# Kernel optimization log

Hardware: AMD Instinct MI355X
Metric: run time of the kernel (lower is better)

Reference implementation:

```python
import jax, jax.numpy as jnp
import numpy as np

TEMP = 0.2
L_MAIN, L_VIEW, L_SUP, L_UNSUP = 1.0, 1.0, 1.0, 0.2
N, D, V, P, NEG, U = 100000, 256, 3, 1024, 1024, 2048


def setup_inputs() -> dict:
    key = jax.random.key(0)
    ks = jax.random.split(key, 8)
    fused_logit = jax.random.normal(ks[0], (N,), dtype=jnp.float32)
    view_logits = jax.random.normal(ks[1], (V, N), dtype=jnp.float32)
    proj = jax.random.normal(ks[2], (V, N, D), dtype=jnp.float32)
    proj = proj / jnp.linalg.norm(proj, axis=-1, keepdims=True)  # 'already normalized'
    labels = jax.random.randint(ks[3], (N,), 0, 2).astype(jnp.float32)
    train_mask = jax.random.randint(ks[4], (N,), 0, 2).astype(bool)
    train_pos_idx = jax.random.randint(ks[5], (P,), 0, N)
    train_neg_idx = jax.random.randint(ks[6], (NEG,), 0, N)
    unlabeled_idx = jax.random.randint(ks[7], (U,), 0, N)  # len == max_unsup_samples -> no subsampling
    return dict(fused_logit=fused_logit, view_logits=view_logits, proj=proj,
                labels=labels, train_mask=train_mask, train_pos_idx=train_pos_idx,
                train_neg_idx=train_neg_idx, unlabeled_idx=unlabeled_idx)


def _masked_bce(logits, labels, mask):
    # BCEWithLogitsLoss mean over masked elements (stable formulation)
    bce = jnp.maximum(logits, 0) - logits * labels + jnp.log1p(jnp.exp(-jnp.abs(logits)))
    mf = mask.astype(logits.dtype)
    return jnp.sum(bce * mf) / jnp.maximum(jnp.sum(mf), 1.0)


def _sup_contrastive(proj, pos_idx, neg_idx, temp):
    lab_idx = jnp.concatenate([pos_idx, neg_idx])
    node_labels = jnp.concatenate([jnp.ones(pos_idx.shape[0]), jnp.zeros(neg_idx.shape[0])])
    L = lab_idx.shape[0]
    Vv = proj.shape[0]
    z = proj[:, lab_idx, :].transpose(1, 0, 2)          # [L, V, D]
    zf = z.reshape(L * Vv, -1)                           # [L*V, D]
    sim = (zf @ zf.T) / temp                             # [L*V, L*V]
    sim = sim - jax.lax.stop_gradient(sim.max(axis=1, keepdims=True))
    es = jnp.exp(sim)
    node = jnp.repeat(jnp.arange(L), Vv)
    view = jnp.tile(jnp.arange(Vv), L)
    flab = jnp.repeat(node_labels, Vv)
    sn = node[:, None] == node[None, :]
    sv = view[:, None] == view[None, :]
    sl = flab[:, None] == flab[None, :]
    eye = jnp.eye(L * Vv, dtype=bool)
    pos_m = ((sn & ~sv) | (~sn & sl)) & ~eye
    neg_m = (~sn) & (~sl) & ~eye
    den_m = pos_m | neg_m
    denom = jnp.sum(es * den_m.astype(es.dtype), axis=1) + 1e-12
    posf = pos_m.astype(es.dtype)
    log_prob = -jnp.log((es * posf + 1e-12) / denom[:, None])
    pos_count = pos_m.sum(axis=1)
    loss_per_anchor = jnp.sum(log_prob * posf, axis=1) / (pos_count.astype(es.dtype) + 1e-12)
    valid = ((pos_count > 0) & (den_m.sum(axis=1) > 0)).astype(es.dtype)
    return jnp.sum(loss_per_anchor * valid) / jnp.maximum(jnp.sum(valid), 1.0)


def _unsup_consistency(proj, unl_idx, temp):
    # Vectorized form of the double python loop: full cosine-sim matrix with
    # masked denominator (all but self) and positives = same node, other views.
    Vv = proj.shape[0]
    z = proj[:, unl_idx, :].transpose(1, 0, 2)           # [U, V, D]
    Uu = z.shape[0]
    M = Uu * Vv
    zf = z.reshape(M, -1)
    zn = zf / (jnp.linalg.norm(zf, axis=1, keepdims=True) + 1e-8)
    es = jnp.exp((zn @ zn.T) / temp)                     # [M, M]
    denom = es.sum(axis=1) - jnp.diag(es) + 1e-12        # exclude self
    node = jnp.repeat(jnp.arange(Uu), Vv)
    view = jnp.tile(jnp.arange(Vv), Uu)
    pos_m = (node[:, None] == node[None, :]) & (view[:, None] != view[None, :])
    posf = pos_m.astype(es.dtype)
    log_prob = -jnp.log(es / denom[:, None])
    per_anchor = jnp.sum(log_prob * posf, axis=1) / (Vv - 1)
    return jnp.mean(per_anchor)


def reference(fused_logit, view_logits, proj, labels, train_mask,
              train_pos_idx, train_neg_idx, unlabeled_idx):
    main_loss = _masked_bce(fused_logit, labels, train_mask)
    view_loss = jnp.mean(jax.vmap(lambda lg: _masked_bce(lg, labels, train_mask))(view_logits))
    sup_loss = _sup_contrastive(proj, train_pos_idx, train_neg_idx, TEMP)
    unsup_loss = _unsup_consistency(proj, unlabeled_idx, TEMP)
    total = L_MAIN * main_loss + L_VIEW * view_loss + L_SUP * sup_loss + L_UNSUP * unsup_loss
    return jnp.stack([total, main_loss, view_loss, sup_loss, unsup_loss])
```

## Files before the change

### kernel.cpp

```cpp
#include <hip/hip_runtime.h>
#include <math.h>

typedef short short8 __attribute__((ext_vector_type(8)));
typedef float floatx4 __attribute__((ext_vector_type(4)));

#define TEMP_INV 5.0f
#define W_UNSUP 0.2f
#define NB_BCE 256
#define NSPLIT 4

static __device__ __forceinline__ unsigned short f2bf(float f) {
  unsigned int u = __float_as_uint(f);
  u += 0x7FFFu + ((u >> 16) & 1u);
  return (unsigned short)(u >> 16);
}

__device__ __forceinline__ float block_sum256(float v) {
  __shared__ float sh[4];
  for (int m = 1; m <= 32; m <<= 1) v += __shfl_xor(v, m);
  __syncthreads();
  if ((threadIdx.x & 63) == 0) sh[threadIdx.x >> 6] = v;
  __syncthreads();
  return sh[0] + sh[1] + sh[2] + sh[3];
}

__global__ void detect_kernel(const unsigned int* __restrict__ w, int nw, int* __restrict__ flag) {
  __shared__ int s_int, s_flt;
  if (threadIdx.x == 0) { s_int = 1; s_flt = 1; }
  __syncthreads();
  for (int i = threadIdx.x; i < nw; i += blockDim.x) {
    unsigned int x = w[i];
    if (x != 0u && x != 1u) s_int = 0;
    if (x != 0u && x != 0x3F800000u) s_flt = 0;
  }
  __syncthreads();
  if (threadIdx.x == 0) *flag = s_int ? 0 : (s_flt ? 1 : 2);
}

__global__ __launch_bounds__(256) void bce_kernel(
    const float* __restrict__ fused, const float* __restrict__ viewl,
    const float* __restrict__ labels, const void* __restrict__ maskp,
    const int* __restrict__ flagp, float* __restrict__ partials, int N, int V) {
  const int flag = *flagp;
  float cnt = 0.f, sm = 0.f;
  float sv[8];
  for (int v = 0; v < 8; v++) sv[v] = 0.f;
  const int Vc = V > 8 ? 8 : V;
  for (int i = blockIdx.x * blockDim.x + threadIdx.x; i < N; i += gridDim.x * blockDim.x) {
    bool m;
    if (flag == 0)      m = ((const int*)maskp)[i] != 0;
    else if (flag == 1) m = ((const float*)maskp)[i] != 0.0f;
    else                m = ((const unsigned char*)maskp)[i] != 0;
    if (!m) continue;
    float y = labels[i];
    cnt += 1.0f;
    float x = fused[i];
    sm += fmaxf(x, 0.f) - x * y + log1pf(__expf(-fabsf(x)));
    for (int v = 0; v < Vc; v++) {
      float xv = viewl[(size_t)v * N + i];
      sv[v] += fmaxf(xv, 0.f) - xv * y + log1pf(__expf(-fabsf(xv)));
    }
  }
  float tot = block_sum256(cnt);
  if (threadIdx.x == 0) partials[blockIdx.x * 16 + 0] = tot;
  tot = block_sum256(sm);
  if (threadIdx.x == 0) partials[blockIdx.x * 16 + 1] = tot;
  for (int v = 0; v < Vc; v++) {
    tot = block_sum256(sv[v]);
    if (threadIdx.x == 0) partials[blockIdx.x * 16 + 2 + v] = tot;
  }
}

__global__ __launch_bounds__(256) void gather_kernel(
    const float* __restrict__ proj, const int* __restrict__ pos_idx,
    const int* __restrict__ neg_idx, const int* __restrict__ unl_idx,
    unsigned short* __restrict__ zsup, unsigned short* __restrict__ zuns,
    float* __restrict__ dsup, float* __restrict__ duns,
    int N, int D, int V, int P, int Msup, int Muns) {
  const int prob = blockIdx.y;
  const int r = blockIdx.x;
  const int M = prob ? Muns : Msup;
  if (r >= M) return;
  const int l = r / V, v = r - l * V;
  const int idx = prob ? unl_idx[l] : (l < P ? pos_idx[l] : neg_idx[l - P]);
  const float* src = proj + ((size_t)v * N + (size_t)idx) * D;
  const int t = threadIdx.x;
  float s = 0.f;
  for (int d = t; d < D; d += blockDim.x) { float x = src[d]; s += x * x; }
  for (int m = 1; m <= 32; m <<= 1) s += __shfl_xor(s, m);
  __shared__ float sh[4];
  if ((t & 63) == 0) sh[t >> 6] = s;
  __syncthreads();
  const float n2 = sh[0] + sh[1] + sh[2] + sh[3];
  if (prob == 0) {
    for (int d = t; d < D; d += blockDim.x) zsup[(size_t)r * D + d] = f2bf(src[d]);
    if (t == 0) dsup[r] = n2 * TEMP_INV;
  } else {
    const float sc = 1.0f / (sqrtf(n2) + 1e-8f);
    for (int d = t; d < D; d += blockDim.x) zuns[(size_t)r * D + d] = f2bf(src[d] * sc);
    if (t == 0) duns[r] = n2 * sc * sc * TEMP_INV;
  }
}

__global__ __launch_bounds__(256) void sim_kernel(
    const unsigned short* __restrict__ zsup, const unsigned short* __restrict__ zuns,
    float* __restrict__ Esup, float* __restrict__ Bsup,
    float* __restrict__ Euns, float* __restrict__ Buns,
    int Msup, int Muns, int PV, int V) {
  const int prob = blockIdx.z;
  const unsigned short* __restrict__ z = prob ? zuns : zsup;
  float* __restrict__ Ep = prob ? Euns : Esup;
  float* __restrict__ Bp = prob ? Buns : Bsup;
  const int M = prob ? Muns : Msup;

  const int tid = threadIdx.x;
  const int lane = tid & 63;
  const int wave = tid >> 6;
  const int q = lane >> 4;
  const int n16 = lane & 15;

  const int rowBase = blockIdx.y * 64 + wave * 16;

  int arow = rowBase + n16; if (arow >= M) arow = M - 1;
  short8 afrag[8];
  {
    const unsigned short* zr = z + (size_t)arow * 256 + q * 8;
#pragma unroll
    for (int ks = 0; ks < 8; ks++) afrag[ks] = *(const short8*)(zr + ks * 32);
  }

  int bs[4], be[4];
#pragma unroll
  for (int r = 0; r < 4; r++) {
    int row = rowBase + q * 4 + r;
    if (row >= M) row = M - 1;
    if (prob == 0) { bs[r] = (row < PV) ? 0 : PV; be[r] = (row < PV) ? PV : M; }
    else           { int b0 = (row / V) * V; bs[r] = b0; be[r] = b0 + V; }
  }

  float Eacc[4] = {0.f, 0.f, 0.f, 0.f};
  float Bacc[4] = {0.f, 0.f, 0.f, 0.f};

  __shared__ __align__(16) unsigned short lds[64 * 264];

  int cps = ((M + NSPLIT * 64 - 1) / (NSPLIT * 64)) * 64;
  int colStart = blockIdx.x * cps;
  int colEnd = colStart + cps; if (colEnd > M) colEnd = M;

  for (int c0 = colStart; c0 < colEnd; c0 += 64) {
    __syncthreads();
#pragma unroll
    for (int cc = 0; cc < 8; cc++) {
      int chunk = cc * 256 + tid;
      int rrow = chunk >> 5;
      int off = (chunk & 31) * 8;
      int gcol = c0 + rrow;
      short8 vv = {0, 0, 0, 0, 0, 0, 0, 0};
      if (gcol < M) vv = *(const short8*)(z + (size_t)gcol * 256 + off);
      *(short8*)(&lds[rrow * 264 + off]) = vv;
    }
    __syncthreads();

#pragma unroll
    for (int cb = 0; cb < 4; cb++) {
      floatx4 acc = {0.f, 0.f, 0.f, 0.f};
      const unsigned short* bp = &lds[(cb * 16 + n16) * 264 + q * 8];
#pragma unroll
      for (int ks = 0; ks < 8; ks++) {
        short8 bfrag = *(const short8*)(bp + ks * 32);
        acc = __builtin_amdgcn_mfma_f32_16x16x32_bf16(afrag[ks], bfrag, acc, 0, 0, 0);
      }
      int j = c0 + cb * 16 + n16;
      if (j < M) {
#pragma unroll
        for (int r = 0; r < 4; r++) {
          float t = acc[r] * TEMP_INV;
          Eacc[r] += __expf(t - 5.0f);
          Bacc[r] += (j >= bs[r] && j < be[r]) ? t : 0.0f;
        }
      }
    }
  }

#pragma unroll
  for (int r = 0; r < 4; r++) {
    float e = Eacc[r], b = Bacc[r];
    for (int m = 1; m <= 8; m <<= 1) { e += __shfl_xor(e, m); b += __shfl_xor(b, m); }
    int row = rowBase + q * 4 + r;
    if (n16 == 0 && row < M) {
      Ep[(size_t)blockIdx.x * M + row] = e;
      Bp[(size_t)blockIdx.x * M + row] = b;
    }
  }
}

__global__ __launch_bounds__(256) void finalize_kernel(
    const float* __restrict__ partials,
    const float* __restrict__ Esup, const float* __restrict__ Bsup, const float* __restrict__ dsup,
    const float* __restrict__ Euns, const float* __restrict__ Buns, const float* __restrict__ duns,
    int Msup, int Muns, int PV, int P, int NEG, int V, float* __restrict__ out) {
  const int t = threadIdx.x;
  float cnt = 0.f, sm = 0.f, sv[8];
  for (int v = 0; v < 8; v++) sv[v] = 0.f;
  const int Vc = V > 8 ? 8 : V;
  for (int b = t; b < NB_BCE; b += 256) {
    cnt += partials[b * 16 + 0];
    sm  += partials[b * 16 + 1];
    for (int v = 0; v < Vc; v++) sv[v] += partials[b * 16 + 2 + v];
  }
  cnt = block_sum256(cnt);
  sm = block_sum256(sm);
  float svt = 0.f;
  for (int v = 0; v < Vc; v++) svt += block_sum256(sv[v]);
  const float denomC = fmaxf(cnt, 1.0f);
  const float main_loss = sm / denomC;
  const float view_loss = (svt / denomC) / (float)V;

  float ssup = 0.f;
  for (int row = t; row < Msup; row += 256) {
    float E = 0.f, B = 0.f;
    for (int s = 0; s < NSPLIT; s++) {
      E += Esup[(size_t)s * Msup + row];
      B += Bsup[(size_t)s * Msup + row];
    }
    float d = dsup[row];
    float dn = E - __expf(d - 5.0f);
    float cl = (row < PV) ? (float)P : (float)NEG;
    float pc = (float)(V - 1) + (cl - 1.0f) * (float)V;
    ssup += logf(dn) + 5.0f - (B - d) / pc;
  }
  ssup = block_sum256(ssup);
  const float sup_loss = ssup / (float)Msup;

  float suns = 0.f;
  for (int row = t; row < Muns; row += 256) {
    float E = 0.f, B = 0.f;
    for (int s = 0; s < NSPLIT; s++) {
      E += Euns[(size_t)s * Muns + row];
      B += Buns[(size_t)s * Muns + row];
    }
    float d = duns[row];
    float dn = E - __expf(d - 5.0f);
    suns += logf(dn) + 5.0f - (B - d) / (float)(V - 1);
  }
  suns = block_sum256(suns);
  const float unsup_loss = suns / (float)Muns;

  if (t == 0) {
    float total = main_loss + view_loss + sup_loss + W_UNSUP * unsup_loss;
    out[0] = total;
    out[1] = main_loss;
    out[2] = view_loss;
    out[3] = sup_loss;
    out[4] = unsup_loss;
  }
}

extern "C" void kernel_launch(void* const* d_in, const int* in_sizes, int n_in,
                              void* d_out, int out_size, void* d_ws, size_t ws_size,
                              hipStream_t stream) {
  const float* fused  = (const float*)d_in[0];
  const float* viewl  = (const float*)d_in[1];
  const float* proj   = (const float*)d_in[2];
  const float* labels = (const float*)d_in[3];
  const void*  maskp  = d_in[4];
  const int* pos_idx  = (const int*)d_in[5];
  const int* neg_idx  = (const int*)d_in[6];
  const int* unl_idx  = (const int*)d_in[7];

  const int N = in_sizes[0];
  const int V = in_sizes[1] / N;
  const int D = in_sizes[2] / in_sizes[1];
  const int P = in_sizes[5];
  const int NEG = in_sizes[6];
  const int U = in_sizes[7];
  const int L = P + NEG;
  const int Msup = L * V;
  const int Muns = U * V;
  const int PV = P * V;

  char* ws = (char*)d_ws;
  size_t off = 0;
  auto alloc = [&](size_t bytes) { size_t o = off; off += (bytes + 255) & ~(size_t)255; return o; };
  const size_t o_flag = alloc(4);
  const size_t o_part = alloc((size_t)NB_BCE * 16 * 4);
  const size_t o_zsup = alloc((size_t)Msup * D * 2);
  const size_t o_zuns = alloc((size_t)Muns * D * 2);
  const size_t o_dsup = alloc((size_t)Msup * 4);
  const size_t o_duns = alloc((size_t)Muns * 4);
  const size_t o_Esup = alloc((size_t)NSPLIT * Msup * 4);
  const size_t o_Bsup = alloc((size_t)NSPLIT * Msup * 4);
  const size_t o_Euns = alloc((size_t)NSPLIT * Muns * 4);
  const size_t o_Buns = alloc((size_t)NSPLIT * Muns * 4);

  int* flag = (int*)(ws + o_flag);
  float* partials = (float*)(ws + o_part);
  unsigned short* zsup = (unsigned short*)(ws + o_zsup);
  unsigned short* zuns = (unsigned short*)(ws + o_zuns);
  float* dsup = (float*)(ws + o_dsup);
  float* duns = (float*)(ws + o_duns);
  float* Esup = (float*)(ws + o_Esup);
  float* Bsup = (float*)(ws + o_Bsup);
  float* Euns = (float*)(ws + o_Euns);
  float* Buns = (float*)(ws + o_Buns);

  int nw = N / 4 < 256 ? N / 4 : 256;
  detect_kernel<<<1, 256, 0, stream>>>((const unsigned int*)maskp, nw, flag);
  bce_kernel<<<NB_BCE, 256, 0, stream>>>(fused, viewl, labels, maskp, flag, partials, N, V);

  const int Mmax = Msup > Muns ? Msup : Muns;
  dim3 ggrid(Mmax, 2);
  gather_kernel<<<ggrid, 256, 0, stream>>>(proj, pos_idx, neg_idx, unl_idx,
                                           zsup, zuns, dsup, duns, N, D, V, P, Msup, Muns);

  dim3 sgrid(NSPLIT, (Mmax + 63) / 64, 2);
  sim_kernel<<<sgrid, 256, 0, stream>>>(zsup, zuns, Esup, Bsup, Euns, Buns, Msup, Muns, PV, V);

  finalize_kernel<<<1, 256, 0, stream>>>(partials, Esup, Bsup, dsup, Euns, Buns, duns,
                                         Msup, Muns, PV, P, NEG, V, (float*)d_out);
}
```

Measured before the change: 480.5 us.

## Exploit Gram matrix symmetry with upper-triangular tiles and atomic row/column sums

The similarity kernel now launches one block per upper-triangular 64x64 tile of the symmetric Gram matrix and adds each tile's exp and positive-mask sums to both its rows and its columns. Partial sums are reduced in LDS, then atomically added to global per-row accumulators that the gather kernel zeroes first. This roughly halves the MFMA and exp work and drops the NSPLIT partial buffers, at the cost of atomics and nondeterministic summation order. The gather kernel also processes eight rows per block with one warp-sized group per row and vectorized loads.

Result: slower. 496.6 us (+3.3%).

```diff
diff --git a/kernel.cpp b/kernel.cpp
--- a/kernel.cpp
+++ b/kernel.cpp
@@ -7,7 +7,6 @@
 #define TEMP_INV 5.0f
 #define W_UNSUP 0.2f
 #define NB_BCE 256
-#define NSPLIT 4
 
 static __device__ __forceinline__ unsigned short f2bf(float f) {
   unsigned int u = __float_as_uint(f);
@@ -76,120 +75,185 @@
     const int* __restrict__ neg_idx, const int* __restrict__ unl_idx,
     unsigned short* __restrict__ zsup, unsigned short* __restrict__ zuns,
     float* __restrict__ dsup, float* __restrict__ duns,
+    float* __restrict__ Esup, float* __restrict__ Bsup,
+    float* __restrict__ Euns, float* __restrict__ Buns,
     int N, int D, int V, int P, int Msup, int Muns) {
   const int prob = blockIdx.y;
-  const int r = blockIdx.x;
   const int M = prob ? Muns : Msup;
+  const int r0 = blockIdx.x * 8;
+  const int t = threadIdx.x;
+  if (t < 8) {
+    int rz = r0 + t;
+    if (rz < M) {
+      if (prob) { Euns[rz] = 0.f; Buns[rz] = 0.f; }
+      else      { Esup[rz] = 0.f; Bsup[rz] = 0.f; }
+    }
+  }
+  const int sub = t >> 5, ln = t & 31;
+  const int r = r0 + sub;
   if (r >= M) return;
   const int l = r / V, v = r - l * V;
   const int idx = prob ? unl_idx[l] : (l < P ? pos_idx[l] : neg_idx[l - P]);
-  const float* src = proj + ((size_t)v * N + (size_t)idx) * D;
-  const int t = threadIdx.x;
+  const float* src = proj + ((size_t)v * N + (size_t)idx) * D + ln * 8;
+  floatx4 p0 = *(const floatx4*)(src);
+  floatx4 p1 = *(const floatx4*)(src + 4);
   float s = 0.f;
-  for (int d = t; d < D; d += blockDim.x) { float x = src[d]; s += x * x; }
-  for (int m = 1; m <= 32; m <<= 1) s += __shfl_xor(s, m);
-  __shared__ float sh[4];
-  if ((t & 63) == 0) sh[t >> 6] = s;
-  __syncthreads();
-  const float n2 = sh[0] + sh[1] + sh[2] + sh[3];
-  if (prob == 0) {
-    for (int d = t; d < D; d += blockDim.x) zsup[(size_t)r * D + d] = f2bf(src[d]);
-    if (t == 0) dsup[r] = n2 * TEMP_INV;
-  } else {
-    const float sc = 1.0f / (sqrtf(n2) + 1e-8f);
-    for (int d = t; d < D; d += blockDim.x) zuns[(size_t)r * D + d] = f2bf(src[d] * sc);
-    if (t == 0) duns[r] = n2 * sc * sc * TEMP_INV;
-  }
+#pragma unroll
+  for (int k = 0; k < 4; k++) s += p0[k] * p0[k] + p1[k] * p1[k];
+  for (int m = 1; m <= 16; m <<= 1) s += __shfl_xor(s, m);
+  const float n2 = s;
+  float sc = 1.0f, dval = n2 * TEMP_INV;
+  if (prob) {
+    sc = 1.0f / (sqrtf(n2) + 1e-8f);
+    dval = n2 * sc * sc * TEMP_INV;
+  }
+  short8 vv;
+#pragma unroll
+  for (int k = 0; k < 4; k++) {
+    vv[k]     = (short)f2bf(p0[k] * sc);
+    vv[k + 4] = (short)f2bf(p1[k] * sc);
+  }
+  unsigned short* zd = prob ? zuns : zsup;
+  *(short8*)(zd + (size_t)r * 256 + ln * 8) = vv;
+  if (ln == 0) (prob ? duns : dsup)[r] = dval;
 }
 
 __global__ __launch_bounds__(256) void sim_kernel(
     const unsigned short* __restrict__ zsup, const unsigned short* __restrict__ zuns,
     float* __restrict__ Esup, float* __restrict__ Bsup,
     float* __restrict__ Euns, float* __restrict__ Buns,
-    int Msup, int Muns, int PV, int V) {
-  const int prob = blockIdx.z;
+    int Msup, int Muns, int PV, int V,
+    int Tsup, int Tuns, int nsSup, int nsUns) {
+  const int prob = blockIdx.y;
   const unsigned short* __restrict__ z = prob ? zuns : zsup;
   float* __restrict__ Ep = prob ? Euns : Esup;
   float* __restrict__ Bp = prob ? Buns : Bsup;
   const int M = prob ? Muns : Msup;
-
+  const int ns = prob ? nsUns : nsSup;
+  const int T = prob ? Tuns : Tsup;
+  const int t = blockIdx.x;
+  if (t >= T) return;
+
+#define TRI_BASE(s) ((s) * ns - ((s) * ((s) - 1)) / 2)
+  int si = (int)((2.0f * ns + 1.0f -
+                  sqrtf((2.0f * ns + 1.0f) * (2.0f * ns + 1.0f) - 8.0f * (float)t)) * 0.5f);
+  if (si < 0) si = 0;
+  if (si > ns - 1) si = ns - 1;
+  while (si > 0 && TRI_BASE(si) > t) si--;
+  while (si < ns - 1 && TRI_BASE(si + 1) <= t) si++;
+  const int sj = si + (t - TRI_BASE(si));
+#undef TRI_BASE
+
+  const int R0 = si * 64, C0 = sj * 64;
   const int tid = threadIdx.x;
-  const int lane = tid & 63;
   const int wave = tid >> 6;
-  const int q = lane >> 4;
-  const int n16 = lane & 15;
-
-  const int rowBase = blockIdx.y * 64 + wave * 16;
-
-  int arow = rowBase + n16; if (arow >= M) arow = M - 1;
-  short8 afrag[8];
-  {
-    const unsigned short* zr = z + (size_t)arow * 256 + q * 8;
-#pragma unroll
-    for (int ks = 0; ks < 8; ks++) afrag[ks] = *(const short8*)(zr + ks * 32);
-  }
-
-  int bs[4], be[4];
-#pragma unroll
-  for (int r = 0; r < 4; r++) {
-    int row = rowBase + q * 4 + r;
+  const int wr = wave >> 1, wc = wave & 1;
+  const int q = (tid >> 4) & 3;
+  const int n16 = tid & 15;
+
+  __shared__ __align__(16) unsigned short lds[64 * 264];
+  __shared__ float redRE[64], redRB[64], redCE[64], redCB[64];
+
+#pragma unroll
+  for (int cc = 0; cc < 8; cc++) {
+    int chunk = cc * 256 + tid;
+    int rrow = chunk >> 5;
+    int off = (chunk & 31) * 8;
+    int gcol = C0 + rrow;
+    short8 vv = {0, 0, 0, 0, 0, 0, 0, 0};
+    if (gcol < M) vv = *(const short8*)(z + (size_t)gcol * 256 + off);
+    *(short8*)(&lds[rrow * 264 + off]) = vv;
+  }
+  if (tid < 64) { redRE[tid] = 0.f; redRB[tid] = 0.f; redCE[tid] = 0.f; redCB[tid] = 0.f; }
+
+  short8 a[2][8];
+#pragma unroll
+  for (int m = 0; m < 2; m++) {
+    int row = R0 + wr * 32 + m * 16 + n16;
     if (row >= M) row = M - 1;
-    if (prob == 0) { bs[r] = (row < PV) ? 0 : PV; be[r] = (row < PV) ? PV : M; }
-    else           { int b0 = (row / V) * V; bs[r] = b0; be[r] = b0 + V; }
-  }
-
-  float Eacc[4] = {0.f, 0.f, 0.f, 0.f};
-  float Bacc[4] = {0.f, 0.f, 0.f, 0.f};
-
-  __shared__ __align__(16) unsigned short lds[64 * 264];
-
-  int cps = ((M + NSPLIT * 64 - 1) / (NSPLIT * 64)) * 64;
-  int colStart = blockIdx.x * cps;
-  int colEnd = colStart + cps; if (colEnd > M) colEnd = M;
-
-  for (int c0 = colStart; c0 < colEnd; c0 += 64) {
-    __syncthreads();
-#pragma unroll
-    for (int cc = 0; cc < 8; cc++) {
-      int chunk = cc * 256 + tid;
-      int rrow = chunk >> 5;
-      int off = (chunk & 31) * 8;
-      int gcol = c0 + rrow;
-      short8 vv = {0, 0, 0, 0, 0, 0, 0, 0};
-      if (gcol < M) vv = *(const short8*)(z + (size_t)gcol * 256 + off);
-      *(short8*)(&lds[rrow * 264 + off]) = vv;
-    }
-    __syncthreads();
-
-#pragma unroll
-    for (int cb = 0; cb < 4; cb++) {
-      floatx4 acc = {0.f, 0.f, 0.f, 0.f};
-      const unsigned short* bp = &lds[(cb * 16 + n16) * 264 + q * 8];
-#pragma unroll
-      for (int ks = 0; ks < 8; ks++) {
-        short8 bfrag = *(const short8*)(bp + ks * 32);
-        acc = __builtin_amdgcn_mfma_f32_16x16x32_bf16(afrag[ks], bfrag, acc, 0, 0, 0);
-      }
-      int j = c0 + cb * 16 + n16;
-      if (j < M) {
-#pragma unroll
-        for (int r = 0; r < 4; r++) {
-          float t = acc[r] * TEMP_INV;
-          Eacc[r] += __expf(t - 5.0f);
-          Bacc[r] += (j >= bs[r] && j < be[r]) ? t : 0.0f;
-        }
-      }
-    }
-  }
-
-#pragma unroll
-  for (int r = 0; r < 4; r++) {
-    float e = Eacc[r], b = Bacc[r];
-    for (int m = 1; m <= 8; m <<= 1) { e += __shfl_xor(e, m); b += __shfl_xor(b, m); }
-    int row = rowBase + q * 4 + r;
-    if (n16 == 0 && row < M) {
-      Ep[(size_t)blockIdx.x * M + row] = e;
-      Bp[(size_t)blockIdx.x * M + row] = b;
+    const unsigned short* zr = z + (size_t)row * 256 + q * 8;
+#pragma unroll
+    for (int ks = 0; ks < 8; ks++) a[m][ks] = *(const short8*)(zr + ks * 32);
+  }
+
+  int bs[2][4], be[2][4];
+#pragma unroll
+  for (int m = 0; m < 2; m++)
+#pragma unroll
+    for (int r = 0; r < 4; r++) {
+      int row = R0 + wr * 32 + m * 16 + q * 4 + r;
+      if (row >= M) row = M - 1;
+      if (prob == 0) { bs[m][r] = row < PV ? 0 : PV; be[m][r] = row < PV ? PV : M; }
+      else           { int b0 = (row / V) * V; bs[m][r] = b0; be[m][r] = b0 + V; }
+    }
+
+  __syncthreads();
+
+  floatx4 acc00 = {0.f, 0.f, 0.f, 0.f}, acc01 = {0.f, 0.f, 0.f, 0.f};
+  floatx4 acc10 = {0.f, 0.f, 0.f, 0.f}, acc11 = {0.f, 0.f, 0.f, 0.f};
+#pragma unroll
+  for (int ks = 0; ks < 8; ks++) {
+    const unsigned short* bp = &lds[(wc * 32 + n16) * 264 + q * 8 + ks * 32];
+    short8 b0 = *(const short8*)bp;
+    short8 b1 = *(const short8*)(bp + 16 * 264);
+    acc00 = __builtin_amdgcn_mfma_f32_16x16x32_bf16(a[0][ks], b0, acc00, 0, 0, 0);
+    acc01 = __builtin_amdgcn_mfma_f32_16x16x32_bf16(a[0][ks], b1, acc01, 0, 0, 0);
+    acc10 = __builtin_amdgcn_mfma_f32_16x16x32_bf16(a[1][ks], b0, acc10, 0, 0, 0);
+    acc11 = __builtin_amdgcn_mfma_f32_16x16x32_bf16(a[1][ks], b1, acc11, 0, 0, 0);
+  }
+
+  float er0[4] = {0, 0, 0, 0}, er1[4] = {0, 0, 0, 0};
+  float br0[4] = {0, 0, 0, 0}, br1[4] = {0, 0, 0, 0};
+  float ec0 = 0.f, ec1 = 0.f, bc0 = 0.f, bc1 = 0.f;
+  const int j0 = C0 + wc * 32 + n16;
+  const int j1 = j0 + 16;
+
+#define EPI(ACC, MM, JN, ECOL, BCOL, ERA, BRA)                        \
+  _Pragma("unroll")                                                   \
+  for (int r = 0; r < 4; r++) {                                       \
+    int row = R0 + wr * 32 + MM * 16 + q * 4 + r;                     \
+    float tv = ACC[r] * TEMP_INV;                                     \
+    bool valid = (row < M) && (JN < M);                               \
+    float e = valid ? __expf(tv - 5.0f) : 0.0f;                       \
+    float bv = (valid && JN >= bs[MM][r] && JN < be[MM][r]) ? tv : 0.0f; \
+    ERA[r] += e; BRA[r] += bv; ECOL += e; BCOL += bv;                 \
+  }
+  EPI(acc00, 0, j0, ec0, bc0, er0, br0)
+  EPI(acc01, 0, j1, ec1, bc1, er0, br0)
+  EPI(acc10, 1, j0, ec0, bc0, er1, br1)
+  EPI(acc11, 1, j1, ec1, bc1, er1, br1)
+#undef EPI
+
+#pragma unroll
+  for (int mr = 0; mr < 8; mr++) {
+    const int m = mr >> 2, r = mr & 3;
+    float e = m ? er1[r] : er0[r];
+    float b = m ? br1[r] : br0[r];
+    for (int msk = 1; msk <= 8; msk <<= 1) { e += __shfl_xor(e, msk); b += __shfl_xor(b, msk); }
+    if (n16 == 0) {
+      int lr = wr * 32 + m * 16 + q * 4 + r;
+      atomicAdd(&redRE[lr], e);
+      atomicAdd(&redRB[lr], b);
+    }
+  }
+  if (si != sj) {
+    float e = ec0, b = bc0;
+    e += __shfl_xor(e, 16); e += __shfl_xor(e, 32);
+    b += __shfl_xor(b, 16); b += __shfl_xor(b, 32);
+    if (q == 0) { atomicAdd(&redCE[wc * 32 + n16], e); atomicAdd(&redCB[wc * 32 + n16], b); }
+    e = ec1; b = bc1;
+    e += __shfl_xor(e, 16); e += __shfl_xor(e, 32);
+    b += __shfl_xor(b, 16); b += __shfl_xor(b, 32);
+    if (q == 0) { atomicAdd(&redCE[wc * 32 + 16 + n16], e); atomicAdd(&redCB[wc * 32 + 16 + n16], b); }
+  }
+
+  __syncthreads();
+  if (tid < 64) {
+    int row = R0 + tid;
+    if (row < M) { atomicAdd(&Ep[row], redRE[tid]); atomicAdd(&Bp[row], redRB[tid]); }
+    if (si != sj) {
+      int col = C0 + tid;
+      if (col < M) { atomicAdd(&Ep[col], redCE[tid]); atomicAdd(&Bp[col], redCB[tid]); }
     }
   }
 }
@@ -218,11 +282,7 @@
 
   float ssup = 0.f;
   for (int row = t; row < Msup; row += 256) {
-    float E = 0.f, B = 0.f;
-    for (int s = 0; s < NSPLIT; s++) {
-      E += Esup[(size_t)s * Msup + row];
-      B += Bsup[(size_t)s * Msup + row];
-    }
+    float E = Esup[row], B = Bsup[row];
     float d = dsup[row];
     float dn = E - __expf(d - 5.0f);
     float cl = (row < PV) ? (float)P : (float)NEG;
@@ -234,11 +294,7 @@
 
   float suns = 0.f;
   for (int row = t; row < Muns; row += 256) {
-    float E = 0.f, B = 0.f;
-    for (int s = 0; s < NSPLIT; s++) {
-      E += Euns[(size_t)s * Muns + row];
-      B += Buns[(size_t)s * Muns + row];
-    }
+    float E = Euns[row], B = Buns[row];
     float d = duns[row];
     float dn = E - __expf(d - 5.0f);
     suns += logf(dn) + 5.0f - (B - d) / (float)(V - 1);
@@ -288,10 +344,10 @@
   const size_t o_zuns = alloc((size_t)Muns * D * 2);
   const size_t o_dsup = alloc((size_t)Msup * 4);
   const size_t o_duns = alloc((size_t)Muns * 4);
-  const size_t o_Esup = alloc((size_t)NSPLIT * Msup * 4);
-  const size_t o_Bsup = alloc((size_t)NSPLIT * Msup * 4);
-  const size_t o_Euns = alloc((size_t)NSPLIT * Muns * 4);
-  const size_t o_Buns = alloc((size_t)NSPLIT * Muns * 4);
+  const size_t o_Esup = alloc((size_t)Msup * 4);
+  const size_t o_Bsup = alloc((size_t)Msup * 4);
+  const size_t o_Euns = alloc((size_t)Muns * 4);
+  const size_t o_Buns = alloc((size_t)Muns * 4);
 
   int* flag = (int*)(ws + o_flag);
   float* partials = (float*)(ws + o_part);
@@ -309,12 +365,20 @@
   bce_kernel<<<NB_BCE, 256, 0, stream>>>(fused, viewl, labels, maskp, flag, partials, N, V);
 
   const int Mmax = Msup > Muns ? Msup : Muns;
-  dim3 ggrid(Mmax, 2);
+  dim3 ggrid((Mmax + 7) / 8, 2);
   gather_kernel<<<ggrid, 256, 0, stream>>>(proj, pos_idx, neg_idx, unl_idx,
-                                           zsup, zuns, dsup, duns, N, D, V, P, Msup, Muns);
-
-  dim3 sgrid(NSPLIT, (Mmax + 63) / 64, 2);
-  sim_kernel<<<sgrid, 256, 0, stream>>>(zsup, zuns, Esup, Bsup, Euns, Buns, Msup, Muns, PV, V);
+                                           zsup, zuns, dsup, duns,
+                                           Esup, Bsup, Euns, Buns,
+                                           N, D, V, P, Msup, Muns);
+
+  const int nsS = (Msup + 63) / 64;
+  const int nsU = (Muns + 63) / 64;
+  const int Ts = nsS * (nsS + 1) / 2;
+  const int Tu = nsU * (nsU + 1) / 2;
+  const int Tmax = Ts > Tu ? Ts : Tu;
+  dim3 sgrid(Tmax, 2);
+  sim_kernel<<<sgrid, 256, 0, stream>>>(zsup, zuns, Esup, Bsup, Euns, Buns,
+                                        Msup, Muns, PV, V, Ts, Tu, nsS, nsU);
 
   finalize_kernel<<<1, 256, 0, stream>>>(partials, Esup, Bsup, dsup, Euns, Buns, duns,
                                          Msup, Muns, PV, P, NEG, V, (float*)d_out);
```
